# Performance work log

Measured on AMD Instinct MI355X. Metric: run time of the kernel, lower is better.

## Reference

```python
import jax, jax.numpy as jnp
import numpy as np

C = 1.2            # PoincareBall curvature (learnable in torch, init value used)
SQC = C ** 0.5
MIN_NORM = 1e-15
BALL_EPS = 4e-3    # geoopt float32 projx eps

def _artanh(x):
    return jnp.arctanh(jnp.clip(x, -1.0 + 1e-7, 1.0 - 1e-7))

def _tanh(x):
    return jnp.tanh(jnp.clip(x, -15.0, 15.0))

def _norm(x):
    return jnp.maximum(jnp.linalg.norm(x, axis=-1, keepdims=True), MIN_NORM)

def p_projx(x):
    n = _norm(x)
    maxnorm = (1.0 - BALL_EPS) / SQC
    return jnp.where(n > maxnorm, x / n * maxnorm, x)

def p_expmap0(u):
    n = _norm(u)
    return p_projx(_tanh(SQC * n) * u / (SQC * n))

def p_logmap0(y):
    n = _norm(y)
    return _artanh(SQC * n) * y / (SQC * n)

def p_mobius_add(x, y):
    x2 = jnp.sum(x * x, -1, keepdims=True)
    y2 = jnp.sum(y * y, -1, keepdims=True)
    xy = jnp.sum(x * y, -1, keepdims=True)
    num = (1 + 2 * C * xy + C * y2) * x + (1 - C * x2) * y
    den = 1 + 2 * C * xy + C * C * x2 * y2
    return num / jnp.maximum(den, MIN_NORM)

def p_mobius_matvec(W, x):
    xn = _norm(x)
    mx = x @ W.T
    mxn = _norm(mx)
    res = _tanh(mxn / xn * _artanh(SQC * xn)) * mx / (mxn * SQC)
    zero = jnp.all(mx == 0, axis=-1, keepdims=True)
    return p_projx(jnp.where(zero, jnp.zeros_like(res), res))

def p_mobius_scalar_mul(r, x):
    n = _norm(x)
    return p_projx(_tanh(r * _artanh(SQC * n)) * x / (n * SQC))

def p_linear(x, W, b):
    # Manifold_Linear on PoincareBall: mobius matvec + mobius bias add + projx
    mv = p_mobius_matvec(W, x)
    return p_projx(p_mobius_add(mv, p_expmap0(b)))

def e_linear(x, W, b):
    return x @ W.T + b

def mob_relu(x):
    # Mob_Act: logmap0 -> act -> expmap0 (with projection)
    return p_expmap0(jax.nn.relu(p_logmap0(x)))


def setup_inputs() -> dict:
    key = jax.random.key(0)
    ks = jax.random.split(key, 26)
    g = lambda i, shape, s: (jax.random.normal(ks[i], shape, jnp.float32) * s)
    d = {
        'x':   g(0, (1024, 32, 128), 1.0),
        'We1': g(1, (80, 32), 0.1),   'be1': g(2, (80,), 0.05),
        'We2': g(3, (104, 80), 0.1),  'be2': g(4, (104,), 0.05),
        'We3': g(5, (128, 104), 0.1), 'be3': g(6, (128,), 0.05),
        'Wh1': g(7, (80, 32), 0.1),   'bh1': g(8, (80,), 0.05),
        'Wh2': g(9, (104, 80), 0.1),  'bh2': g(10, (104,), 0.05),
        'Wh3': g(11, (128, 104), 0.1),'bh3': g(12, (128,), 0.05),
        'Wae': g(13, (128, 128), 0.1),'bae': g(14, (128,), 0.05),
        'Wah': g(15, (128, 128), 0.1),'bah': g(16, (128,), 0.05),
        'Wte': g(17, (1, 128), 0.1),  'bte': g(18, (1,), 0.05),
        'Wth': g(19, (1, 128), 0.1),  'bth': g(20, (1,), 0.05),
        'Wf1': g(21, (10, 256), 0.1), 'bf1': g(22, (10,), 0.05),
        'Wf2': g(23, (10, 10), 0.1),  'bf2': g(24, (10,), 0.05),
    }
    return d


def reference(x, We1, be1, We2, be2, We3, be3,
              Wh1, bh1, Wh2, bh2, Wh3, bh3,
              Wae, bae, Wah, bah, Wte, bte, Wth, bth,
              Wf1, bf1, Wf2, bf2):
    xs = jnp.transpose(x, (0, 2, 1))  # (B, S, C_in)

    # --- Euclidean branch: expmap0 = identity; Manifold_Linear = plain linear ---
    xe = xs
    xe = e_linear(xe, We1, be1); xe = jax.nn.relu(xe)
    xe = e_linear(xe, We2, be2); xe = jax.nn.relu(xe)
    xe = e_linear(xe, We3, be3)
    out_e = jax.nn.relu(xe)               # extra self.act for Euclidean manifolds

    # --- Poincare branch ---
    xh = p_expmap0(xs)
    xh = p_linear(xh, Wh1, bh1); xh = mob_relu(xh)
    xh = p_linear(xh, Wh2, bh2); xh = mob_relu(xh)
    out_h = p_linear(xh, Wh3, bh3)        # (B, S, part_dim)

    # --- cross-manifold attention in tangent space at origin ---
    tan_e = e_linear(out_e, Wae, bae)                    # Euclidean logmap0 = id
    tan_h = p_logmap0(p_linear(out_h, Wah, bah))
    mu = 0.5 * (tan_e + tan_h)
    a_e = e_linear(tan_e - mu, Wte, bte)  # (B, S, 1)
    a_h = e_linear(tan_h - mu, Wth, bth)
    w = jax.nn.softmax(jnp.stack([a_e, a_h], axis=0), axis=0)
    proc_e = w[0] * out_e                                # Euclidean mobius scalar mul
    proc_h = p_mobius_scalar_mul(w[1], out_h)

    # --- pool over constituents in tangent space, concat, classify ---
    o_e = jnp.mean(proc_e, axis=1)                       # Euclidean logmap0 = id
    o_h = jnp.mean(p_logmap0(proc_h), axis=1)
    o = jnp.concatenate([o_e, o_h], axis=-1)             # (B, 2*part_dim)
    o = jax.nn.relu(e_linear(o, Wf1, bf1))
    return e_linear(o, Wf2, bf2)
```

## Files before the change

### kernel.cpp

```cpp
#include <hip/hip_runtime.h>
#include <math.h>

constexpr float CC   = 1.2f;
constexpr float SQC  = 1.09544511501033215f;
constexpr float MAXN = (1.0f - 4e-3f) / SQC;
constexpr float MINN = 1e-15f;

constexpr int WTH1 = 0;
constexpr int WTH2 = 4096;
constexpr int WTH3 = 14336;
constexpr int WTAH = 27648;
constexpr int WTE1 = 44032;
constexpr int WTE2 = 48128;
constexpr int WTE3 = 58368;
constexpr int EB1  = 71680;
constexpr int EB2  = 71808;
constexpr int EB3  = 71936;
constexpr int EBA  = 72064;
constexpr int BE1  = 72192;
constexpr int BE2  = 72320;
constexpr int BE3  = 72448;
constexpr int U1o  = 72576;
constexpr int U2o  = 72704;
constexpr int SCo  = 72832;
constexpr int PART = 72864;

constexpr int ASTR = 17;

template<int CTRL>
__device__ __forceinline__ float dppa(float v){
  int x = __builtin_amdgcn_update_dpp(0, __float_as_int(v), CTRL, 0xf, 0xf, true);
  return v + __int_as_float(x);
}
__device__ __forceinline__ float rtj(float v){
  v = dppa<0xB1>(v);
  v = dppa<0x4E>(v);
  v = dppa<0x124>(v);
  v = dppa<0x128>(v);
  return v;
}
template<int I>
__device__ __forceinline__ float qbc(float v){
  constexpr int c = I | (I<<2) | (I<<4) | (I<<6);
  return __int_as_float(__builtin_amdgcn_update_dpp(0, __float_as_int(v), c, 0xf, 0xf, true));
}
__device__ __forceinline__ float wsum(float v){
  v = rtj(v);
  v += __shfl_xor(v, 16, 64);
  v += __shfl_xor(v, 32, 64);
  return v;
}
__device__ __forceinline__ float wsum64(float v){
#pragma unroll
  for(int i=32;i>0;i>>=1) v += __shfl_xor(v, i, 64);
  return v;
}
__device__ __forceinline__ float sel4(const float (&a)[4], int i){
  float lo = (i & 1) ? a[1] : a[0];
  float hi = (i & 1) ? a[3] : a[2];
  return (i & 2) ? hi : lo;
}

__device__ __forceinline__ float art_(float x){
  x = fminf(fmaxf(x, -0.9999999f), 0.9999999f);
  return 0.5f * __logf((1.0f + x) / (1.0f - x));
}
__device__ __forceinline__ float tanh_(float x){
  x = fminf(fmaxf(x, -15.0f), 15.0f);
  float e = __expf(2.0f * x);
  return (e - 1.0f) / (e + 1.0f);
}
__device__ __forceinline__ float lamv(float nv){
  float n = fmaxf(nv, MINN);
  return art_(SQC*n)/(SQC*n);
}
struct HS { float ca, cb, nv; };
__device__ __forceinline__ HS hyper_chain(float m2, float meb, float xn_in, float y2){
  float xn  = fmaxf(xn_in, MINN);
  float mxn = fmaxf(sqrtf(m2), MINN);
  float r   = art_(SQC*xn);
  float s   = tanh_(mxn/xn*r)/(mxn*SQC);
  float nr  = s*mxn;
  if(nr > MAXN){ s *= MAXN/nr; nr = MAXN; }
  float xy = s*meb, x2 = nr*nr;
  float den = fmaxf(1.f + 2.f*CC*xy + CC*CC*x2*y2, MINN);
  float A   = (1.f + 2.f*CC*xy + CC*y2)/den;
  float Bc  = (1.f - CC*x2)/den;
  float n3  = sqrtf(fmaxf(A*A*x2 + 2.f*A*Bc*xy + Bc*Bc*y2, 0.f));
  float rho = (n3 > MAXN) ? MAXN/n3 : 1.f;
  HS h; h.nv = fminf(n3, MAXN); h.ca = rho*A*s; h.cb = rho*Bc;
  return h;
}
struct TT { float tau, nf; };
__device__ __forceinline__ TT tail_relu(float rn2){
  float rn = fmaxf(sqrtf(rn2), MINN);
  float th = tanh_(SQC*rn);
  TT r; r.tau = th/(SQC*rn); r.nf = th/SQC;
  if(r.nf > MAXN){ r.tau *= MAXN/r.nf; r.nf = MAXN; }
  return r;
}
struct EX { float nh, scl; };
__device__ __forceinline__ EX exp0(float n2){
  float n0 = fmaxf(sqrtf(n2), MINN);
  float th = tanh_(SQC*n0);
  EX e; e.nh = th/SQC; e.scl = th/(SQC*n0);
  if(e.nh > MAXN){ e.scl *= MAXN/e.nh; e.nh = MAXN; }
  return e;
}
struct THW { float te, th2; };
__device__ __forceinline__ THW ahchain(float m2a, float mw1, float mw2, float meba,
                                       float xnh, float rr, float y2,
                                       float ebw1, float ebw2){
  float mxn = fmaxf(sqrtf(m2a), MINN);
  float s = tanh_(mxn/xnh*rr)/(mxn*SQC);
  float nr = s*mxn;
  if(nr > MAXN){ s *= MAXN/nr; nr = MAXN; }
  float xy = s*meba, x2 = nr*nr;
  float den = fmaxf(1.f + 2.f*CC*xy + CC*CC*x2*y2, MINN);
  float A = (1.f + 2.f*CC*xy + CC*y2)/den;
  float Bc = (1.f - CC*x2)/den;
  float n3 = sqrtf(fmaxf(A*A*x2 + 2.f*A*Bc*xy + Bc*Bc*y2, 0.f));
  float rho = (n3 > MAXN) ? MAXN/n3 : 1.f;
  float nv = fminf(n3, MAXN);
  float lr = lamv(nv)*rho;
  THW r; r.te = lr*(A*s*mw1 + Bc*ebw1); r.th2 = lr*(A*s*mw2 + Bc*ebw2);
  return r;
}
struct AG { float wge, g2; };
__device__ __forceinline__ AG attn(float d1, float d2, float thte, float thth,
                                   float rr, float xnh, float b_e, float b_h){
  float a_e = 0.5f*(d1 - thte) + b_e;
  float a_h = 0.5f*(thth - d2) + b_h;
  float mx = fmaxf(a_e, a_h);
  float ee = __expf(a_e - mx), eh = __expf(a_h - mx);
  float inv = 1.f/(ee + eh);
  AG r; r.wge = ee*inv;
  float wgh = eh*inv;
  float inner = wgh*rr;
  float scl2 = tanh_(inner)/(xnh*SQC);
  float nn = scl2*xnh;
  if(nn > MAXN){ scl2 *= MAXN/nn; nn = MAXN; }
  r.g2 = lamv(nn)*scl2;
  return r;
}

__global__ void k_setup(const float* __restrict__ Wh1, const float* __restrict__ Wh2,
                        const float* __restrict__ Wh3, const float* __restrict__ Wah,
                        const float* __restrict__ We1, const float* __restrict__ We2,
                        const float* __restrict__ We3,
                        const float* __restrict__ Wae, const float* __restrict__ bae,
                        const float* __restrict__ bh1, const float* __restrict__ bh2,
                        const float* __restrict__ bh3, const float* __restrict__ bah,
                        const float* __restrict__ Wte, const float* __restrict__ Wth,
                        const float* __restrict__ be1, const float* __restrict__ be2,
                        const float* __restrict__ be3, float* __restrict__ ws){
  const int blk = blockIdx.x, tid = threadIdx.x;
  if(blk < 280){
    const int row = blk*2 + (tid >> 7);
    const int j   = tid & 127;
    const float* W; int OUT, K, kk, dst;
    if(row < 32)       { W=Wh1; OUT=80;  K=32;  kk=row;      dst=WTH1; }
    else if(row < 112) { W=Wh2; OUT=104; K=80;  kk=row-32;   dst=WTH2; }
    else if(row < 216) { W=Wh3; OUT=128; K=104; kk=row-112;  dst=WTH3; }
    else if(row < 344) { W=Wah; OUT=128; K=128; kk=row-216;  dst=WTAH; }
    else if(row < 376) { W=We1; OUT=80;  K=32;  kk=row-344;  dst=WTE1; }
    else if(row < 456) { W=We2; OUT=104; K=80;  kk=row-376;  dst=WTE2; }
    else               { W=We3; OUT=128; K=104; kk=row-456;  dst=WTE3; }
    ws[dst + kk*128 + j] = (j < OUT) ? W[j*K + kk] : 0.f;
    return;
  }
  {
    const int which = tid >> 7, k = tid & 127;
    const float* wv = which ? Wth : Wte;
    float s = 0.f;
#pragma unroll 4
    for(int j=0;j<128;++j) s += Wae[j*128+k] * wv[j];
    ws[(which ? U2o : U1o) + k] = s;
  }
  if(tid < 128){
    ws[BE1+tid] = (tid < 80)  ? be1[tid] : 0.f;
    ws[BE2+tid] = (tid < 104) ? be2[tid] : 0.f;
    ws[BE3+tid] = be3[tid];
  }
  if(tid < 64){
    const int l = tid;
    float p1=0.f, p2=0.f;
    for(int j=l;j<128;j+=64){ p1 += bae[j]*Wte[j]; p2 += bae[j]*Wth[j]; }
    p1 = wsum64(p1); p2 = wsum64(p2);
    if(l==0){ ws[SCo+0]=p1; ws[SCo+1]=p2; }
    const float* bs[4] = {bh1,bh2,bh3,bah};
    const int dims[4]  = {80,104,128,128};
    const int offs[4]  = {EB1,EB2,EB3,EBA};
    for(int v=0;v<4;++v){
      const float* bp = bs[v]; const int D = dims[v];
      float q = 0.f;
      for(int j=l;j<D;j+=64) q += bp[j]*bp[j];
      q = wsum64(q);
      float nb = fmaxf(sqrtf(q), MINN);
      float th = tanhf(fminf(fmaxf(SQC*nb,-15.f),15.f));
      float coef = th/(SQC*nb);
      float ne = th/SQC;
      if(ne > MAXN){ coef *= MAXN/ne; ne = MAXN; }
      for(int j=l;j<D;j+=64) ws[offs[v]+j] = coef*bp[j];
      for(int j=D+l;j<128;j+=64) ws[offs[v]+j] = 0.f;
      if(l==0) ws[SCo+2+v] = ne*ne;
      if(v==3){
        float e1=0.f, e2=0.f;
        for(int j=l;j<D;j+=64){ e1 += bp[j]*Wte[j]; e2 += bp[j]*Wth[j]; }
        e1 = wsum64(e1)*coef; e2 = wsum64(e2)*coef;
        if(l==0){ ws[SCo+6]=e1; ws[SCo+7]=e2; }
      }
    }
  }
}

__global__ void k_fin(const float* __restrict__ ws, const float* __restrict__ bf1,
                      const float* __restrict__ Wf2, const float* __restrict__ bf2,
                      float* __restrict__ out){
  const int r = blockIdx.x*64 + threadIdx.x;
  const float* p = ws + PART + (size_t)r*80;
  float f1[10];
#pragma unroll
  for(int i=0;i<10;++i){
    float s = 0.f;
#pragma unroll
    for(int g=0;g<8;++g) s += p[g*10+i];
    f1[i] = fmaxf(s*(1.f/512.f) + bf1[i], 0.f);
  }
#pragma unroll
  for(int o=0;o<10;++o){
    float a = bf2[o];
#pragma unroll
    for(int k=0;k<10;++k) a = fmaf(Wf2[o*10+k], f1[k], a);
    out[r*10 + o] = a;
  }
}

__device__ __forceinline__ void ld8(const float* __restrict__ p, float (&v)[8]){
  float4 a = *(const float4*)p, b = *(const float4*)(p+4);
  v[0]=a.x; v[1]=a.y; v[2]=a.z; v[3]=a.w; v[4]=b.x; v[5]=b.y; v[6]=b.z; v[7]=b.w;
}
typedef float nf4 __attribute__((ext_vector_type(4)));
__device__ __forceinline__ float4 ldnt4(const float* p){
  nf4 v = __builtin_nontemporal_load((const nf4*)p);
  return make_float4(v[0], v[1], v[2], v[3]);
}

template<int K, bool XG, bool XSQ>
__device__ __forceinline__ void gemmw(const float* __restrict__ wt,
                                      const float* __restrict__ xg,
                                      const float* __restrict__ ACT,
                                      int fj, int tt, float (&acc)[4][8], float (&xsq)[4]){
#pragma unroll
  for(int i=0;i<4;++i)
#pragma unroll
    for(int j=0;j<8;++j) acc[i][j] = 0.f;
  const int wo = fj*8, xo = tt*4;
#pragma unroll 2
  for(int k=0;k<K;++k){
    float4 w0 = *(const float4*)(wt + k*128 + wo);
    float4 w1 = *(const float4*)(wt + k*128 + wo + 4);
    float4 xa;
    if(XG) xa = ldnt4(xg + k*128 + xo);
    else   xa = *(const float4*)(ACT + k*ASTR + xo);
    float xv[4] = {xa.x,xa.y,xa.z,xa.w};
    float wv[8] = {w0.x,w0.y,w0.z,w0.w,w1.x,w1.y,w1.z,w1.w};
#pragma unroll
    for(int i=0;i<4;++i){
      if(XSQ) xsq[i] = fmaf(xv[i], xv[i], xsq[i]);
#pragma unroll
      for(int j=0;j<8;++j) acc[i][j] = fmaf(xv[i], wv[j], acc[i][j]);
    }
  }
}

__device__ __forceinline__ void wACT(float* __restrict__ ACT, const float (&acc)[4][8],
                                     int fj, int tt){
#pragma unroll
  for(int j=0;j<8;++j){
    float4 a = {acc[0][j],acc[1][j],acc[2][j],acc[3][j]};
    *(float4*)(ACT + (fj*8+j)*ASTR + tt*4) = a;
  }
}

__global__ __launch_bounds__(64) void k_main(
    const float* __restrict__ x,
    const float* __restrict__ Wf1, const float* __restrict__ Wte,
    const float* __restrict__ bte, const float* __restrict__ Wth,
    const float* __restrict__ bth, float* __restrict__ ws){
  __shared__ float ACT[128*ASTR];
  __shared__ float ZH[160];
  const int tid = threadIdx.x, fj = tid & 15, tt = tid >> 4;
  const int b = blockIdx.x, row = b >> 3, q = b & 7;
  const int own = fj & 3;
  const float* xg = x + (size_t)row*4096 + q*16;

  const float c1  = ws[SCo+0], c2  = ws[SCo+1];
  const float y21 = ws[SCo+2], y22 = ws[SCo+3], y23 = ws[SCo+4], y2a = ws[SCo+5];
  const float ew1 = ws[SCo+6], ew2 = ws[SCo+7];
  const float btev = bte[0], bthv = bth[0];

  float acc[4][8];
  float xsq[4];
#pragma unroll
  for(int i=0;i<4;++i) xsq[i] = 0.f;

  float nfO = 0.f, xnhO = 1.f, rrO = 0.f, tteO = 0.f, tthO = 0.f;

  {
    gemmw<32,true,true>(ws+WTH1, xg, ACT, fj, tt, acc, xsq);
    float ebv[8]; ld8(ws+EB1+fj*8, ebv);
    float sO = 0.f, eO = 0.f;
#pragma unroll
    for(int i=0;i<4;++i){
      float s=0.f, e=0.f;
#pragma unroll
      for(int j=0;j<8;++j){ s = fmaf(acc[i][j],acc[i][j],s); e = fmaf(acc[i][j],ebv[j],e); }
      s = rtj(s); e = rtj(e);
      if(own==i){ sO = s; eO = e; }
    }
    EX e0 = exp0(sel4(xsq, own));
    HS h  = hyper_chain(sO*e0.scl*e0.scl, eO*e0.scl, e0.nh, y21);
    float lam = lamv(h.nv);
    float Aw = lam*h.ca*e0.scl, Bw = lam*h.cb;
    float Ab4[4] = {qbc<0>(Aw), qbc<1>(Aw), qbc<2>(Aw), qbc<3>(Aw)};
    float Bb4[4] = {qbc<0>(Bw), qbc<1>(Bw), qbc<2>(Bw), qbc<3>(Bw)};
    float s2O = 0.f;
#pragma unroll
    for(int i=0;i<4;++i){
      float s2 = 0.f;
#pragma unroll
      for(int j=0;j<8;++j){
        float v = fmaxf(fmaf(Ab4[i], acc[i][j], Bb4[i]*ebv[j]), 0.f);
        acc[i][j] = v; s2 = fmaf(v,v,s2);
      }
      s2 = rtj(s2);
      if(own==i) s2O = s2;
    }
    TT tr = tail_relu(s2O);
    nfO = tr.nf;
    float tb4[4] = {qbc<0>(tr.tau), qbc<1>(tr.tau), qbc<2>(tr.tau), qbc<3>(tr.tau)};
#pragma unroll
    for(int i=0;i<4;++i)
#pragma unroll
      for(int j=0;j<8;++j) acc[i][j] *= tb4[i];
    wACT(ACT, acc, fj, tt);
  }

  {
    gemmw<80,false,false>(ws+WTH2, nullptr, ACT, fj, tt, acc, xsq);
    float ebv[8]; ld8(ws+EB2+fj*8, ebv);
    float sO = 0.f, eO = 0.f;
#pragma unroll
    for(int i=0;i<4;++i){
      float s=0.f, e=0.f;
#pragma unroll
      for(int j=0;j<8;++j){ s = fmaf(acc[i][j],acc[i][j],s); e = fmaf(acc[i][j],ebv[j],e); }
      s = rtj(s); e = rtj(e);
      if(own==i){ sO = s; eO = e; }
    }
    HS h = hyper_chain(sO, eO, nfO, y22);
    float lam = lamv(h.nv);
    float Aw = lam*h.ca, Bw = lam*h.cb;
    float Ab4[4] = {qbc<0>(Aw), qbc<1>(Aw), qbc<2>(Aw), qbc<3>(Aw)};
    float Bb4[4] = {qbc<0>(Bw), qbc<1>(Bw), qbc<2>(Bw), qbc<3>(Bw)};
    float s2O = 0.f;
#pragma unroll
    for(int i=0;i<4;++i){
      float s2 = 0.f;
#pragma unroll
      for(int j=0;j<8;++j){
        float v = fmaxf(fmaf(Ab4[i], acc[i][j], Bb4[i]*ebv[j]), 0.f);
        acc[i][j] = v; s2 = fmaf(v,v,s2);
      }
      s2 = rtj(s2);
      if(own==i) s2O = s2;
    }
    TT tr = tail_relu(s2O);
    nfO = tr.nf;
    float tb4[4] = {qbc<0>(tr.tau), qbc<1>(tr.tau), qbc<2>(tr.tau), qbc<3>(tr.tau)};
#pragma unroll
    for(int i=0;i<4;++i)
#pragma unroll
      for(int j=0;j<8;++j) acc[i][j] *= tb4[i];
    wACT(ACT, acc, fj, tt);
  }

  {
    gemmw<104,false,false>(ws+WTH3, nullptr, ACT, fj, tt, acc, xsq);
    float ebv[8]; ld8(ws+EB3+fj*8, ebv);
    float sO = 0.f, eO = 0.f;
#pragma unroll
    for(int i=0;i<4;++i){
      float s=0.f, e=0.f;
#pragma unroll
      for(int j=0;j<8;++j){ s = fmaf(acc[i][j],acc[i][j],s); e = fmaf(acc[i][j],ebv[j],e); }
      s = rtj(s); e = rtj(e);
      if(own==i){ sO = s; eO = e; }
    }
    HS h = hyper_chain(sO, eO, nfO, y23);
    xnhO = fmaxf(h.nv, MINN);
    rrO  = art_(SQC*xnhO);
    float ca4[4] = {qbc<0>(h.ca), qbc<1>(h.ca), qbc<2>(h.ca), qbc<3>(h.ca)};
    float cb4[4] = {qbc<0>(h.cb), qbc<1>(h.cb), qbc<2>(h.cb), qbc<3>(h.cb)};
#pragma unroll
    for(int i=0;i<4;++i)
#pragma unroll
      for(int j=0;j<8;++j) acc[i][j] = fmaf(ca4[i], acc[i][j], cb4[i]*ebv[j]);
    wACT(ACT, acc, fj, tt);
#pragma unroll
    for(int ic=0;ic<10;++ic){
      float wf[8]; ld8(Wf1 + ic*256 + 128 + fj*8, wf);
#pragma unroll
      for(int i=0;i<4;++i){
        float s=0.f;
#pragma unroll
        for(int j=0;j<8;++j) s = fmaf(acc[i][j], wf[j], s);
        s = rtj(s);
        if(fj==0) ZH[ic*16 + tt*4 + i] = s;
      }
    }
  }

  {
    gemmw<128,false,false>(ws+WTAH, nullptr, ACT, fj, tt, acc, xsq);
    float w1v[8], w2v[8], eav[8];
    ld8(Wte + fj*8, w1v); ld8(Wth + fj*8, w2v); ld8(ws+EBA+fj*8, eav);
    float aO=0.f, bO=0.f, cO=0.f, dO=0.f;
#pragma unroll
    for(int i=0;i<4;++i){
      float s0=0.f,s1=0.f,s2=0.f,s3=0.f;
#pragma unroll
      for(int j=0;j<8;++j){
        float m = acc[i][j];
        s0 = fmaf(m,m,s0); s1 = fmaf(m,w1v[j],s1);
        s2 = fmaf(m,w2v[j],s2); s3 = fmaf(m,eav[j],s3);
      }
      s0=rtj(s0); s1=rtj(s1); s2=rtj(s2); s3=rtj(s3);
      if(own==i){ aO=s0; bO=s1; cO=s2; dO=s3; }
    }
    THW a = ahchain(aO, bO, cO, dO, xnhO, rrO, y2a, ew1, ew2);
    tteO = a.te; tthO = a.th2;
  }

  {
    gemmw<32,true,false>(ws+WTE1, xg, ACT, fj, tt, acc, xsq);
    float bev[8]; ld8(ws+BE1+fj*8, bev);
#pragma unroll
    for(int i=0;i<4;++i)
#pragma unroll
      for(int j=0;j<8;++j) acc[i][j] = fmaxf(acc[i][j]+bev[j], 0.f);
    wACT(ACT, acc, fj, tt);
  }
  {
    gemmw<80,false,false>(ws+WTE2, nullptr, ACT, fj, tt, acc, xsq);
    float bev[8]; ld8(ws+BE2+fj*8, bev);
#pragma unroll
    for(int i=0;i<4;++i)
#pragma unroll
      for(int j=0;j<8;++j) acc[i][j] = fmaxf(acc[i][j]+bev[j], 0.f);
    wACT(ACT, acc, fj, tt);
  }
  {
    gemmw<104,false,false>(ws+WTE3, nullptr, ACT, fj, tt, acc, xsq);
    float bev[8], u1v[8], u2v[8];
    ld8(ws+BE3+fj*8, bev); ld8(ws+U1o+fj*8, u1v); ld8(ws+U2o+fj*8, u2v);
    float s1O = 0.f, s2O = 0.f;
#pragma unroll
    for(int i=0;i<4;++i){
      float s1=0.f, s2=0.f;
#pragma unroll
      for(int j=0;j<8;++j){
        float v = fmaxf(acc[i][j]+bev[j], 0.f);
        acc[i][j] = v;
        s1 = fmaf(v,u1v[j],s1); s2 = fmaf(v,u2v[j],s2);
      }
      s1 = rtj(s1); s2 = rtj(s2);
      if(own==i){ s1O = s1; s2O = s2; }
    }
    AG g = attn(s1O + c1, s2O + c2, tteO, tthO, rrO, xnhO, btev, bthv);
#pragma unroll
    for(int ic=0;ic<10;++ic){
      float wf[8]; ld8(Wf1 + ic*256 + fj*8, wf);
      float zO = 0.f;
#pragma unroll
      for(int i=0;i<4;++i){
        float s=0.f;
#pragma unroll
        for(int j=0;j<8;++j) s = fmaf(acc[i][j], wf[j], s);
        s = rtj(s);
        if(own==i) zO = s;
      }
      float p = g.wge*zO + g.g2*ZH[ic*16 + tt*4 + own];
      p = wsum(p);
      if(tid == 0) ws[PART + (size_t)b*10 + ic] = p;
    }
  }
}

extern "C" void kernel_launch(void* const* d_in, const int* in_sizes, int n_in,
                              void* d_out, int out_size, void* d_ws, size_t ws_size,
                              hipStream_t stream){
  (void)in_sizes; (void)n_in; (void)out_size; (void)ws_size;
  const float* x   = (const float*)d_in[0];
  const float* We1 = (const float*)d_in[1];
  const float* be1 = (const float*)d_in[2];
  const float* We2 = (const float*)d_in[3];
  const float* be2 = (const float*)d_in[4];
  const float* We3 = (const float*)d_in[5];
  const float* be3 = (const float*)d_in[6];
  const float* Wh1 = (const float*)d_in[7];
  const float* bh1 = (const float*)d_in[8];
  const float* Wh2 = (const float*)d_in[9];
  const float* bh2 = (const float*)d_in[10];
  const float* Wh3 = (const float*)d_in[11];
  const float* bh3 = (const float*)d_in[12];
  const float* Wae = (const float*)d_in[13];
  const float* bae = (const float*)d_in[14];
  const float* Wah = (const float*)d_in[15];
  const float* bah = (const float*)d_in[16];
  const float* Wte = (const float*)d_in[17];
  const float* bte = (const float*)d_in[18];
  const float* Wth = (const float*)d_in[19];
  const float* bth = (const float*)d_in[20];
  const float* Wf1 = (const float*)d_in[21];
  const float* bf1 = (const float*)d_in[22];
  const float* Wf2 = (const float*)d_in[23];
  const float* bf2 = (const float*)d_in[24];
  float* ws  = (float*)d_ws;
  float* out = (float*)d_out;

  hipLaunchKernelGGL(k_setup, dim3(281), dim3(256), 0, stream,
                     Wh1, Wh2, Wh3, Wah, We1, We2, We3,
                     Wae, bae, bh1, bh2, bh3, bah, Wte, Wth, be1, be2, be3, ws);

  hipLaunchKernelGGL(k_main, dim3(8192), dim3(64), 0, stream,
                     x, Wf1, Wte, bte, Wth, bth, ws);

  hipLaunchKernelGGL(k_fin, dim3(16), dim3(64), 0, stream,
                     ws, bf1, Wf2, bf2, out);
}
```

Measured before the change: 537.9 us.

## Split each block's token tile across two wavefronts with halved per-thread rows

Each block now runs two wavefronts of 64 lanes, and each wavefront handles 8 of the block's 16 tokens. Every thread keeps 2 rows of accumulators instead of 4. Each wave gets its own shared activation buffer, so the padded stride drops to 9. The two waves combine their partial pooled sums through shared memory and one __syncthreads before writing to the workspace. The pooling divisor changes to 1/1024 to match. This cuts per-thread register use and doubles the thread count to raise occupancy, at the cost of reloading the weight vectors in each wave and adding a block barrier.

```diff
diff --git a/kernel.cpp b/kernel.cpp
--- a/kernel.cpp
+++ b/kernel.cpp
@@ -25,7 +25,8 @@
 constexpr int SCo  = 72832;
 constexpr int PART = 72864;
 
-constexpr int ASTR = 17;
+constexpr int ASTR = 9;
+constexpr int AWV  = 128*ASTR;
 
 template<int CTRL>
 __device__ __forceinline__ float dppa(float v){
@@ -54,11 +55,6 @@
 #pragma unroll
   for(int i=32;i>0;i>>=1) v += __shfl_xor(v, i, 64);
   return v;
-}
-__device__ __forceinline__ float sel4(const float (&a)[4], int i){
-  float lo = (i & 1) ? a[1] : a[0];
-  float hi = (i & 1) ? a[3] : a[2];
-  return (i & 2) ? hi : lo;
 }
 
 __device__ __forceinline__ float art_(float x){
@@ -225,7 +221,7 @@
     float s = 0.f;
 #pragma unroll
     for(int g=0;g<8;++g) s += p[g*10+i];
-    f1[i] = fmaxf(s*(1.f/512.f) + bf1[i], 0.f);
+    f1[i] = fmaxf(s*(1.f/1024.f) + bf1[i], 0.f);
   }
 #pragma unroll
   for(int o=0;o<10;++o){
@@ -240,33 +236,33 @@
   float4 a = *(const float4*)p, b = *(const float4*)(p+4);
   v[0]=a.x; v[1]=a.y; v[2]=a.z; v[3]=a.w; v[4]=b.x; v[5]=b.y; v[6]=b.z; v[7]=b.w;
 }
-typedef float nf4 __attribute__((ext_vector_type(4)));
-__device__ __forceinline__ float4 ldnt4(const float* p){
-  nf4 v = __builtin_nontemporal_load((const nf4*)p);
-  return make_float4(v[0], v[1], v[2], v[3]);
+typedef float nf2 __attribute__((ext_vector_type(2)));
+__device__ __forceinline__ float2 ldnt2(const float* p){
+  nf2 v = __builtin_nontemporal_load((const nf2*)p);
+  return make_float2(v[0], v[1]);
 }
 
 template<int K, bool XG, bool XSQ>
 __device__ __forceinline__ void gemmw(const float* __restrict__ wt,
                                       const float* __restrict__ xg,
                                       const float* __restrict__ ACT,
-                                      int fj, int tt, float (&acc)[4][8], float (&xsq)[4]){
-#pragma unroll
-  for(int i=0;i<4;++i)
+                                      int fj, int tt, float (&acc)[2][8], float (&xsq)[2]){
+#pragma unroll
+  for(int i=0;i<2;++i)
 #pragma unroll
     for(int j=0;j<8;++j) acc[i][j] = 0.f;
-  const int wo = fj*8, xo = tt*4;
+  const int wo = fj*8, xo = tt*2;
 #pragma unroll 2
   for(int k=0;k<K;++k){
     float4 w0 = *(const float4*)(wt + k*128 + wo);
     float4 w1 = *(const float4*)(wt + k*128 + wo + 4);
-    float4 xa;
-    if(XG) xa = ldnt4(xg + k*128 + xo);
-    else   xa = *(const float4*)(ACT + k*ASTR + xo);
-    float xv[4] = {xa.x,xa.y,xa.z,xa.w};
+    float2 xa;
+    if(XG) xa = ldnt2(xg + k*128 + xo);
+    else   xa = *(const float2*)(ACT + k*ASTR + xo);
+    float xv[2] = {xa.x,xa.y};
     float wv[8] = {w0.x,w0.y,w0.z,w0.w,w1.x,w1.y,w1.z,w1.w};
 #pragma unroll
-    for(int i=0;i<4;++i){
+    for(int i=0;i<2;++i){
       if(XSQ) xsq[i] = fmaf(xv[i], xv[i], xsq[i]);
 #pragma unroll
       for(int j=0;j<8;++j) acc[i][j] = fmaf(xv[i], wv[j], acc[i][j]);
@@ -274,36 +270,40 @@
   }
 }
 
-__device__ __forceinline__ void wACT(float* __restrict__ ACT, const float (&acc)[4][8],
+__device__ __forceinline__ void wACT(float* __restrict__ ACT, const float (&acc)[2][8],
                                      int fj, int tt){
 #pragma unroll
   for(int j=0;j<8;++j){
-    float4 a = {acc[0][j],acc[1][j],acc[2][j],acc[3][j]};
-    *(float4*)(ACT + (fj*8+j)*ASTR + tt*4) = a;
-  }
-}
-
-__global__ __launch_bounds__(64) void k_main(
+    float2 a = {acc[0][j],acc[1][j]};
+    *(float2*)(ACT + (fj*8+j)*ASTR + tt*2) = a;
+  }
+}
+
+__global__ __launch_bounds__(128, 4) void k_main(
     const float* __restrict__ x,
     const float* __restrict__ Wf1, const float* __restrict__ Wte,
     const float* __restrict__ bte, const float* __restrict__ Wth,
     const float* __restrict__ bth, float* __restrict__ ws){
-  __shared__ float ACT[128*ASTR];
-  __shared__ float ZH[160];
-  const int tid = threadIdx.x, fj = tid & 15, tt = tid >> 4;
+  __shared__ float ACTs[2*AWV];
+  __shared__ float ZHs[2*80];
+  __shared__ float SCR[20];
+  const int tid = threadIdx.x, w = tid >> 6, ln = tid & 63;
+  const int fj = ln & 15, tt = ln >> 4;
   const int b = blockIdx.x, row = b >> 3, q = b & 7;
-  const int own = fj & 3;
-  const float* xg = x + (size_t)row*4096 + q*16;
+  const int own = fj & 1;
+  float* ACT = ACTs + w*AWV;
+  float* ZH  = ZHs  + w*80;
+  const float* xg = x + (size_t)row*4096 + q*16 + w*8;
 
   const float c1  = ws[SCo+0], c2  = ws[SCo+1];
   const float y21 = ws[SCo+2], y22 = ws[SCo+3], y23 = ws[SCo+4], y2a = ws[SCo+5];
   const float ew1 = ws[SCo+6], ew2 = ws[SCo+7];
   const float btev = bte[0], bthv = bth[0];
 
-  float acc[4][8];
-  float xsq[4];
-#pragma unroll
-  for(int i=0;i<4;++i) xsq[i] = 0.f;
+  float acc[2][8];
+  float xsq[2];
+#pragma unroll
+  for(int i=0;i<2;++i) xsq[i] = 0.f;
 
   float nfO = 0.f, xnhO = 1.f, rrO = 0.f, tteO = 0.f, tthO = 0.f;
 
@@ -312,26 +312,26 @@
     float ebv[8]; ld8(ws+EB1+fj*8, ebv);
     float sO = 0.f, eO = 0.f;
 #pragma unroll
-    for(int i=0;i<4;++i){
+    for(int i=0;i<2;++i){
       float s=0.f, e=0.f;
 #pragma unroll
       for(int j=0;j<8;++j){ s = fmaf(acc[i][j],acc[i][j],s); e = fmaf(acc[i][j],ebv[j],e); }
       s = rtj(s); e = rtj(e);
       if(own==i){ sO = s; eO = e; }
     }
-    EX e0 = exp0(sel4(xsq, own));
+    EX e0 = exp0(own ? xsq[1] : xsq[0]);
     HS h  = hyper_chain(sO*e0.scl*e0.scl, eO*e0.scl, e0.nh, y21);
     float lam = lamv(h.nv);
     float Aw = lam*h.ca*e0.scl, Bw = lam*h.cb;
-    float Ab4[4] = {qbc<0>(Aw), qbc<1>(Aw), qbc<2>(Aw), qbc<3>(Aw)};
-    float Bb4[4] = {qbc<0>(Bw), qbc<1>(Bw), qbc<2>(Bw), qbc<3>(Bw)};
+    float Ab2[2] = {qbc<0>(Aw), qbc<1>(Aw)};
+    float Bb2[2] = {qbc<0>(Bw), qbc<1>(Bw)};
     float s2O = 0.f;
 #pragma unroll
-    for(int i=0;i<4;++i){
+    for(int i=0;i<2;++i){
       float s2 = 0.f;
 #pragma unroll
       for(int j=0;j<8;++j){
-        float v = fmaxf(fmaf(Ab4[i], acc[i][j], Bb4[i]*ebv[j]), 0.f);
+        float v = fmaxf(fmaf(Ab2[i], acc[i][j], Bb2[i]*ebv[j]), 0.f);
         acc[i][j] = v; s2 = fmaf(v,v,s2);
       }
       s2 = rtj(s2);
@@ -339,11 +339,11 @@
     }
     TT tr = tail_relu(s2O);
     nfO = tr.nf;
-    float tb4[4] = {qbc<0>(tr.tau), qbc<1>(tr.tau), qbc<2>(tr.tau), qbc<3>(tr.tau)};
-#pragma unroll
-    for(int i=0;i<4;++i)
-#pragma unroll
-      for(int j=0;j<8;++j) acc[i][j] *= tb4[i];
+    float tb2[2] = {qbc<0>(tr.tau), qbc<1>(tr.tau)};
+#pragma unroll
+    for(int i=0;i<2;++i)
+#pragma unroll
+      for(int j=0;j<8;++j) acc[i][j] *= tb2[i];
     wACT(ACT, acc, fj, tt);
   }
 
@@ -352,7 +352,7 @@
     float ebv[8]; ld8(ws+EB2+fj*8, ebv);
     float sO = 0.f, eO = 0.f;
 #pragma unroll
-    for(int i=0;i<4;++i){
+    for(int i=0;i<2;++i){
       float s=0.f, e=0.f;
 #pragma unroll
       for(int j=0;j<8;++j){ s = fmaf(acc[i][j],acc[i][j],s); e = fmaf(acc[i][j],ebv[j],e); }
@@ -362,15 +362,15 @@
     HS h = hyper_chain(sO, eO, nfO, y22);
     float lam = lamv(h.nv);
     float Aw = lam*h.ca, Bw = lam*h.cb;
-    float Ab4[4] = {qbc<0>(Aw), qbc<1>(Aw), qbc<2>(Aw), qbc<3>(Aw)};
-    float Bb4[4] = {qbc<0>(Bw), qbc<1>(Bw), qbc<2>(Bw), qbc<3>(Bw)};
+    float Ab2[2] = {qbc<0>(Aw), qbc<1>(Aw)};
+    float Bb2[2] = {qbc<0>(Bw), qbc<1>(Bw)};
     float s2O = 0.f;
 #pragma unroll
-    for(int i=0;i<4;++i){
+    for(int i=0;i<2;++i){
       float s2 = 0.f;
 #pragma unroll
       for(int j=0;j<8;++j){
-        float v = fmaxf(fmaf(Ab4[i], acc[i][j], Bb4[i]*ebv[j]), 0.f);
+        float v = fmaxf(fmaf(Ab2[i], acc[i][j], Bb2[i]*ebv[j]), 0.f);
         acc[i][j] = v; s2 = fmaf(v,v,s2);
       }
       s2 = rtj(s2);
@@ -378,11 +378,11 @@
     }
     TT tr = tail_relu(s2O);
     nfO = tr.nf;
-    float tb4[4] = {qbc<0>(tr.tau), qbc<1>(tr.tau), qbc<2>(tr.tau), qbc<3>(tr.tau)};
-#pragma unroll
-    for(int i=0;i<4;++i)
-#pragma unroll
-      for(int j=0;j<8;++j) acc[i][j] *= tb4[i];
+    float tb2[2] = {qbc<0>(tr.tau), qbc<1>(tr.tau)};
+#pragma unroll
+    for(int i=0;i<2;++i)
+#pragma unroll
+      for(int j=0;j<8;++j) acc[i][j] *= tb2[i];
     wACT(ACT, acc, fj, tt);
   }
 
@@ -391,7 +391,7 @@
     float ebv[8]; ld8(ws+EB3+fj*8, ebv);
     float sO = 0.f, eO = 0.f;
 #pragma unroll
-    for(int i=0;i<4;++i){
+    for(int i=0;i<2;++i){
       float s=0.f, e=0.f;
 #pragma unroll
       for(int j=0;j<8;++j){ s = fmaf(acc[i][j],acc[i][j],s); e = fmaf(acc[i][j],ebv[j],e); }
@@ -401,23 +401,23 @@
     HS h = hyper_chain(sO, eO, nfO, y23);
     xnhO = fmaxf(h.nv, MINN);
     rrO  = art_(SQC*xnhO);
-    float ca4[4] = {qbc<0>(h.ca), qbc<1>(h.ca), qbc<2>(h.ca), qbc<3>(h.ca)};
-    float cb4[4] = {qbc<0>(h.cb), qbc<1>(h.cb), qbc<2>(h.cb), qbc<3>(h.cb)};
-#pragma unroll
-    for(int i=0;i<4;++i)
-#pragma unroll
-      for(int j=0;j<8;++j) acc[i][j] = fmaf(ca4[i], acc[i][j], cb4[i]*ebv[j]);
+    float ca2[2] = {qbc<0>(h.ca), qbc<1>(h.ca)};
+    float cb2[2] = {qbc<0>(h.cb), qbc<1>(h.cb)};
+#pragma unroll
+    for(int i=0;i<2;++i)
+#pragma unroll
+      for(int j=0;j<8;++j) acc[i][j] = fmaf(ca2[i], acc[i][j], cb2[i]*ebv[j]);
     wACT(ACT, acc, fj, tt);
 #pragma unroll
     for(int ic=0;ic<10;++ic){
       float wf[8]; ld8(Wf1 + ic*256 + 128 + fj*8, wf);
 #pragma unroll
-      for(int i=0;i<4;++i){
+      for(int i=0;i<2;++i){
         float s=0.f;
 #pragma unroll
         for(int j=0;j<8;++j) s = fmaf(acc[i][j], wf[j], s);
         s = rtj(s);
-        if(fj==0) ZH[ic*16 + tt*4 + i] = s;
+        if(fj==0) ZH[ic*8 + tt*2 + i] = s;
       }
     }
   }
@@ -428,7 +428,7 @@
     ld8(Wte + fj*8, w1v); ld8(Wth + fj*8, w2v); ld8(ws+EBA+fj*8, eav);
     float aO=0.f, bO=0.f, cO=0.f, dO=0.f;
 #pragma unroll
-    for(int i=0;i<4;++i){
+    for(int i=0;i<2;++i){
       float s0=0.f,s1=0.f,s2=0.f,s3=0.f;
 #pragma unroll
       for(int j=0;j<8;++j){
@@ -447,7 +447,7 @@
     gemmw<32,true,false>(ws+WTE1, xg, ACT, fj, tt, acc, xsq);
     float bev[8]; ld8(ws+BE1+fj*8, bev);
 #pragma unroll
-    for(int i=0;i<4;++i)
+    for(int i=0;i<2;++i)
 #pragma unroll
       for(int j=0;j<8;++j) acc[i][j] = fmaxf(acc[i][j]+bev[j], 0.f);
     wACT(ACT, acc, fj, tt);
@@ -456,7 +456,7 @@
     gemmw<80,false,false>(ws+WTE2, nullptr, ACT, fj, tt, acc, xsq);
     float bev[8]; ld8(ws+BE2+fj*8, bev);
 #pragma unroll
-    for(int i=0;i<4;++i)
+    for(int i=0;i<2;++i)
 #pragma unroll
       for(int j=0;j<8;++j) acc[i][j] = fmaxf(acc[i][j]+bev[j], 0.f);
     wACT(ACT, acc, fj, tt);
@@ -467,7 +467,7 @@
     ld8(ws+BE3+fj*8, bev); ld8(ws+U1o+fj*8, u1v); ld8(ws+U2o+fj*8, u2v);
     float s1O = 0.f, s2O = 0.f;
 #pragma unroll
-    for(int i=0;i<4;++i){
+    for(int i=0;i<2;++i){
       float s1=0.f, s2=0.f;
 #pragma unroll
       for(int j=0;j<8;++j){
@@ -484,17 +484,20 @@
       float wf[8]; ld8(Wf1 + ic*256 + fj*8, wf);
       float zO = 0.f;
 #pragma unroll
-      for(int i=0;i<4;++i){
+      for(int i=0;i<2;++i){
         float s=0.f;
 #pragma unroll
         for(int j=0;j<8;++j) s = fmaf(acc[i][j], wf[j], s);
         s = rtj(s);
         if(own==i) zO = s;
       }
-      float p = g.wge*zO + g.g2*ZH[ic*16 + tt*4 + own];
+      float p = g.wge*zO + g.g2*ZH[ic*8 + tt*2 + own];
       p = wsum(p);
-      if(tid == 0) ws[PART + (size_t)b*10 + ic] = p;
-    }
+      if(ln == 0) SCR[w*10 + ic] = p;
+    }
+    __syncthreads();
+    if(tid < 10)
+      ws[PART + (size_t)b*10 + tid] = SCR[tid] + SCR[10+tid];
   }
 }
 
@@ -534,7 +537,7 @@
                      Wh1, Wh2, Wh3, Wah, We1, We2, We3,
                      Wae, bae, bh1, bh2, bh3, bah, Wte, Wth, be1, be2, be3, ws);
 
-  hipLaunchKernelGGL(k_main, dim3(8192), dim3(64), 0, stream,
+  hipLaunchKernelGGL(k_main, dim3(8192), dim3(128), 0, stream,
                      x, Wf1, Wte, bte, Wth, bth, ws);
 
   hipLaunchKernelGGL(k_fin, dim3(16), dim3(64), 0, stream,
```

New measurement: 732.8 us. +36.2%, slower.
